# Performance work log

Hardware: AMD Instinct MI355X
Metric: run time of the kernel (lower is better)

## Reference

```python
import jax, jax.numpy as jnp
import numpy as np
from math import pi

N = 20000        # nodes
E = 640000       # edges (avg degree 32)
H = 128          # hidden_channels = num_filters
NB = 3           # num_bond_features
NGS = 50 - NB    # gaussians in smearing (num_gaussians - num_bond_features)
CUT = 10.0       # cutoff
L = 3            # num_interactions
B = 16           # graphs in batch
LOG2 = 0.6931471805599453


def ssp(x):
    # ShiftedSoftplus
    return jax.nn.softplus(x) - LOG2


def setup_inputs() -> dict:
    key = jax.random.key(0)
    ks = jax.random.split(key, 20)
    s = 0.05
    inp = {
        "z": jax.random.randint(ks[0], (N,), 0, 100),
        "pos": jax.random.uniform(ks[1], (N, 3), jnp.float32),
        "batch": jnp.sort(jax.random.randint(ks[2], (N,), 0, B)),
        "edge_index": jax.random.randint(ks[3], (2, E), 0, N),
        "edge_attr": jax.random.uniform(ks[4], (E, NB), jnp.float32),
        # parameters (stacked over L interaction blocks where per-layer)
        "emb": jax.random.normal(ks[5], (100, H), jnp.float32) * s,
        "mlp_w1": jax.random.normal(ks[6], (L, NB + NGS, H), jnp.float32) * s,
        "mlp_b1": jnp.zeros((L, H), jnp.float32),
        "mlp_w2": jax.random.normal(ks[7], (L, H, H), jnp.float32) * s,
        "mlp_b2": jnp.zeros((L, H), jnp.float32),
        "cf1_w": jax.random.normal(ks[8], (L, H, H), jnp.float32) * s,   # lin1, no bias
        "cf2_w": jax.random.normal(ks[9], (L, H, H), jnp.float32) * s,
        "cf2_b": jnp.zeros((L, H), jnp.float32),
        "lin_w": jax.random.normal(ks[10], (L, H, H), jnp.float32) * s,
        "lin_b": jnp.zeros((L, H), jnp.float32),
        "out1_w": jax.random.normal(ks[11], (H, H // 2), jnp.float32) * s,
        "out1_b": jnp.zeros((H // 2,), jnp.float32),
        "out2_w": jax.random.normal(ks[12], (H // 2, 1), jnp.float32) * s,
        "out2_b": jnp.zeros((1,), jnp.float32),
    }
    return inp


def reference(z, pos, batch, edge_index, edge_attr, emb,
              mlp_w1, mlp_b1, mlp_w2, mlp_b2,
              cf1_w, cf2_w, cf2_b, lin_w, lin_b,
              out1_w, out1_b, out2_w, out2_b):
    row, col = edge_index[0], edge_index[1]  # source j, target i
    h = emb[z]                               # [N,H] embedding_e(z)
    # edge_weight = ||pos[row] - pos[col]||
    ew = jnp.linalg.norm(pos[row] - pos[col], axis=-1)  # [E]
    # GaussianSmearing(0, cutoff, NGS)
    offset = jnp.linspace(0.0, CUT, NGS, dtype=jnp.float32)
    coeff = -0.5 / (offset[1] - offset[0]) ** 2
    gs = jnp.exp(coeff * (ew[:, None] - offset[None, :]) ** 2)  # [E,NGS]
    ea = jnp.concatenate([edge_attr, gs], axis=1)  # [E,50]
    # cosine cutoff weight
    C = 0.5 * (jnp.cos(ew * pi / CUT) + 1.0)       # [E]
    for l in range(L):
        # filter MLP on edge features
        W = ssp(ea @ mlp_w1[l] + mlp_b1[l]) @ mlp_w2[l] + mlp_b2[l]  # [E,H]
        W = W * C[:, None]
        xh = h @ cf1_w[l]                    # lin1 (no bias) [N,H]
        msg = xh[row] * W                    # gather-mul [E,H]
        agg = jax.ops.segment_sum(msg, col, num_segments=N)  # scatter-add [N,H]
        xc = agg @ cf2_w[l] + cf2_b[l]       # lin2
        xc = ssp(xc)
        xc = xc @ lin_w[l] + lin_b[l]        # block output lin
        h = h + xc                           # residual
    h = ssp(h @ out1_w + out1_b)             # [N,H/2]
    per_node = h @ out2_w + out2_b           # [N,1]
    out = jax.ops.segment_sum(per_node, batch, num_segments=B)  # readout 'add' -> [B,1]
    return out
```

## Files before the change

### kernel.cpp

```cpp
#include <hip/hip_runtime.h>
#include <hip/hip_bf16.h>

typedef __attribute__((ext_vector_type(8))) short bfrag;
typedef __attribute__((ext_vector_type(4))) float f32x4;

__device__ __forceinline__ float ssp_f(float x) {
    return fmaxf(x, 0.f) + __logf(1.f + __expf(-fabsf(x))) - 0.6931471805599453f;
}

__device__ __forceinline__ unsigned short f2b(float x) {
    __hip_bfloat16 h = __float2bfloat16(x);
    return *(unsigned short*)&h;
}

__global__ void sniff_kernel(const unsigned int* __restrict__ raw, int* __restrict__ flag)
{
    __shared__ int cnt[256];
    const int t = threadIdx.x;
    unsigned int w = raw[t];
    unsigned int e = (w >> 7) & 0xFFu;
    cnt[t] = (e >= 100u && e <= 135u) ? 1 : 0;
    __syncthreads();
    for (int s = 128; s > 0; s >>= 1) {
        if (t < s) cnt[t] += cnt[t + s];
        __syncthreads();
    }
    if (t == 0) *flag = (cnt[0] >= 160) ? 1 : 0;
}

__global__ void sniff_int_kernel(const unsigned int* __restrict__ z, int* __restrict__ iflag)
{
    __shared__ int cnt[128];
    const int t = threadIdx.x;
    cnt[t] = (z[2 * t + 1] == 0u) ? 1 : 0;
    __syncthreads();
    for (int s = 64; s > 0; s >>= 1) {
        if (t < s) cnt[t] += cnt[t + s];
        __syncthreads();
    }
    if (t == 0) *iflag = (cnt[0] >= 126) ? 1 : 0;
}

struct Cvt16 {
    const void* src[16];
    long off[17];
};

__global__ __launch_bounds__(256) void convert_fused_kernel(
    Cvt16 args, float* __restrict__ F, long total, const int* __restrict__ flag)
{
    long i = (long)blockIdx.x * 256 + threadIdx.x;
    if (i >= total) return;
    int lo = 0, hi = 16;
    while (hi - lo > 1) {
        int mid = (lo + hi) >> 1;
        if (i >= args.off[mid]) lo = mid; else hi = mid;
    }
    long loc = i - args.off[lo];
    if (*flag) F[i] = __bfloat162float(((const __hip_bfloat16*)args.src[lo])[loc]);
    else       F[i] = ((const float*)args.src[lo])[loc];
}

__global__ __launch_bounds__(256) void convert_int_kernel(
    const void* __restrict__ src, int* __restrict__ dst, int n,
    const int* __restrict__ iflag)
{
    int i = blockIdx.x * 256 + threadIdx.x;
    if (i >= n) return;
    if (*iflag) dst[i] = (int)(((const long long*)src)[i]);
    else        dst[i] = ((const int*)src)[i];
}

__global__ __launch_bounds__(256) void embed_kernel(
    const int* __restrict__ z, const float* __restrict__ embf,
    float* __restrict__ h, int NH)
{
    int idx = blockIdx.x * 256 + threadIdx.x;
    if (idx >= NH) return;
    h[idx] = embf[z[idx >> 7] * 128 + (idx & 127)];
}

__global__ __launch_bounds__(256) void zero_int_kernel(int* p, int n)
{
    int i = blockIdx.x * 256 + threadIdx.x;
    if (i < n) p[i] = 0;
}

__global__ __launch_bounds__(256) void hist_kernel(const int* __restrict__ col,
                                                   int* __restrict__ count, int E)
{
    int e = blockIdx.x * 256 + threadIdx.x;
    if (e < E) atomicAdd(&count[col[e]], 1);
}

__global__ __launch_bounds__(256) void scan_kernel(const int* __restrict__ count,
                                                   int* __restrict__ rowptr,
                                                   int* __restrict__ next, int N)
{
    __shared__ int part[256];
    const int t = threadIdx.x;
    const int chunk = (N + 255) / 256;
    const int lo = t * chunk, hi = min(lo + chunk, N);
    int s = 0;
    for (int i = lo; i < hi; ++i) s += count[i];
    part[t] = s;
    __syncthreads();
    if (t == 0) {
        int run = 0;
        for (int i = 0; i < 256; ++i) { int v = part[i]; part[i] = run; run += v; }
        rowptr[N] = run;
    }
    __syncthreads();
    int run = part[t];
    for (int i = lo; i < hi; ++i) {
        rowptr[i] = run; next[i] = run;
        run += count[i];
    }
}

__global__ __launch_bounds__(256) void slot_kernel(const int* __restrict__ col,
                                                   int* __restrict__ next,
                                                   int* __restrict__ slot, int E)
{
    int e = blockIdx.x * 256 + threadIdx.x;
    if (e < E) slot[e] = atomicAdd(&next[col[e]], 1);
}

__global__ __launch_bounds__(256) void perm_kernel(const int* __restrict__ slot,
                                                   int* __restrict__ perm, int E)
{
    int e = blockIdx.x * 256 + threadIdx.x;
    if (e < E) perm[slot[e]] = e;
}

__global__ __launch_bounds__(256) void prep_edges_kernel(
    const float* __restrict__ posf, const int* __restrict__ row,
    const int* __restrict__ col, const float* __restrict__ eattrf,
    const int* __restrict__ perm,
    int* __restrict__ rowS, int* __restrict__ colS,
    float* __restrict__ CS, float* __restrict__ ewS,
    unsigned short* __restrict__ eaS, int E, int NB)
{
    int p = blockIdx.x * 256 + threadIdx.x;
    if (p >= E) return;
    const int e = perm[p];
    const int r = row[e], c = col[e];
    float dx = posf[r*3+0] - posf[c*3+0];
    float dy = posf[r*3+1] - posf[c*3+1];
    float dz = posf[r*3+2] - posf[c*3+2];
    float ew = sqrtf(dx*dx + dy*dy + dz*dz);
    rowS[p] = r; colS[p] = c; ewS[p] = ew;
    CS[p] = 0.5f * (cosf(ew * 0.3141592653589793f) + 1.0f);
    unsigned short* o = eaS + (long)p * 4;
    for (int q = 0; q < 4; ++q)
        o[q] = (q < NB) ? f2b(eattrf[(long)e * NB + q]) : (unsigned short)0;
}

__global__ __launch_bounds__(256) void wtrans_kernel(
    const float* __restrict__ src, unsigned short* __restrict__ dst,
    int K, int Kpad, int N)
{
    int idx = blockIdx.x * 256 + threadIdx.x;
    if (idx >= N * Kpad) return;
    int n = idx / Kpad, k = idx - n * Kpad;
    dst[idx] = (k < K) ? f2b(src[k * N + n]) : (unsigned short)0;
}

__global__ __launch_bounds__(256) void wtrans_node_kernel(
    const float* __restrict__ cf1, const float* __restrict__ cf2,
    const float* __restrict__ lin, unsigned short* __restrict__ dst, int total)
{
    int idx = blockIdx.x * 256 + threadIdx.x;
    if (idx >= total) return;
    int m = idx >> 14;
    int fam = m % 3, l = m / 3;
    int local = idx & 16383;
    int n = local >> 7, k = local & 127;
    const float* src = (fam == 0 ? cf1 : fam == 1 ? cf2 : lin) + (long)l * 16384;
    dst[idx] = f2b(src[k * 128 + n]);
}

template<int MODE>
__global__ __launch_bounds__(256) void node_gemm_tiled(
    const float* __restrict__ in, const float* __restrict__ W,
    const float* __restrict__ bias, float* __restrict__ out, int N)
{
    __shared__ float in_s[32][128];
    const int t = threadIdx.x;
    const long n0 = (long)blockIdx.x * 32;
    for (int i = t; i < 32 * 128; i += 256) {
        long n = n0 + (i >> 7);
        in_s[i >> 7][i & 127] = (n < N) ? in[n * 128 + (i & 127)] : 0.f;
    }
    __syncthreads();
    const int j = t & 31, sub = t >> 5;
    const int c4 = j * 4, rb = sub * 4;
    float acc[4][4];
    float4 bv = make_float4(0.f, 0.f, 0.f, 0.f);
    if (MODE != 0) bv = *(const float4*)(bias + c4);
    #pragma unroll
    for (int i = 0; i < 4; ++i) { acc[i][0]=bv.x; acc[i][1]=bv.y; acc[i][2]=bv.z; acc[i][3]=bv.w; }
    #pragma unroll 4
    for (int k = 0; k < 128; ++k) {
        const float4 wv = *(const float4*)(W + k * 128 + c4);
        #pragma unroll
        for (int i = 0; i < 4; ++i) {
            const float a = in_s[rb + i][k];
            acc[i][0] += a * wv.x; acc[i][1] += a * wv.y;
            acc[i][2] += a * wv.z; acc[i][3] += a * wv.w;
        }
    }
    #pragma unroll
    for (int i = 0; i < 4; ++i) {
        long n = n0 + rb + i;
        if (n >= N) continue;
        float4 o;
        if (MODE == 1) {
            o.x = ssp_f(acc[i][0]); o.y = ssp_f(acc[i][1]);
            o.z = ssp_f(acc[i][2]); o.w = ssp_f(acc[i][3]);
        } else {
            o.x = acc[i][0]; o.y = acc[i][1]; o.z = acc[i][2]; o.w = acc[i][3];
        }
        if (MODE == 2) {
            float4 p = *(const float4*)(out + n * 128 + c4);
            o.x += p.x; o.y += p.y; o.z += p.z; o.w += p.w;
        }
        *(float4*)(out + n * 128 + c4) = o;
    }
}

__global__ __launch_bounds__(256) void node_gemm1_mfma(
    const float* __restrict__ in, const unsigned short* __restrict__ wt,
    float* __restrict__ out, int N)
{
    __shared__ __align__(16) short a_b[32][136];
    const int t = threadIdx.x;
    const long r0 = (long)blockIdx.x * 32;
    for (int i = t; i < 32 * 128; i += 256) {
        const int r = i >> 7, c = i & 127;
        long n = r0 + r;
        a_b[r][c] = (short)f2b((n < N) ? in[n * 128 + c] : 0.f);
    }
    __syncthreads();
    const int lane = t & 63, w = t >> 6;
    const int colL = lane & 15, quad = lane >> 4;
    const int m0 = (w & 1) * 16;
    f32x4 acc[4];
    #pragma unroll
    for (int tt = 0; tt < 4; ++tt) acc[tt] = (f32x4){0.f, 0.f, 0.f, 0.f};
    #pragma unroll
    for (int ks = 0; ks < 4; ++ks) {
        const bfrag a = *(const bfrag*)&a_b[m0 + colL][ks * 32 + quad * 8];
        #pragma unroll
        for (int tt = 0; tt < 4; ++tt) {
            const int n0 = ((w >> 1) * 4 + tt) * 16;
            const bfrag b = *(const bfrag*)&wt[(long)(n0 + colL) * 128 + ks * 32 + quad * 8];
            acc[tt] = __builtin_amdgcn_mfma_f32_16x16x32_bf16(a, b, acc[tt], 0, 0, 0);
        }
    }
    #pragma unroll
    for (int tt = 0; tt < 4; ++tt) {
        const int n0 = ((w >> 1) * 4 + tt) * 16;
        #pragma unroll
        for (int reg = 0; reg < 4; ++reg) {
            long n = r0 + m0 + quad * 4 + reg;
            if (n < N) out[n * 128 + n0 + colL] = acc[tt][reg];
        }
    }
}

__global__ __launch_bounds__(256) void node_gemm23_mfma(
    const float* __restrict__ in,
    const unsigned short* __restrict__ w1t, const float* __restrict__ b1,
    const unsigned short* __restrict__ w2t, const float* __restrict__ b2,
    float* __restrict__ h, int N)
{
    __shared__ __align__(16) short a_b[32][136];
    __shared__ __align__(16) short t_b[32][136];
    const int t = threadIdx.x;
    const long r0 = (long)blockIdx.x * 32;
    for (int i = t; i < 32 * 128; i += 256) {
        const int r = i >> 7, c = i & 127;
        long n = r0 + r;
        a_b[r][c] = (short)f2b((n < N) ? in[n * 128 + c] : 0.f);
    }
    __syncthreads();
    const int lane = t & 63, w = t >> 6;
    const int colL = lane & 15, quad = lane >> 4;
    const int m0 = (w & 1) * 16;
    {
        f32x4 acc[4];
        #pragma unroll
        for (int tt = 0; tt < 4; ++tt) acc[tt] = (f32x4){0.f, 0.f, 0.f, 0.f};
        #pragma unroll
        for (int ks = 0; ks < 4; ++ks) {
            const bfrag a = *(const bfrag*)&a_b[m0 + colL][ks * 32 + quad * 8];
            #pragma unroll
            for (int tt = 0; tt < 4; ++tt) {
                const int n0 = ((w >> 1) * 4 + tt) * 16;
                const bfrag b = *(const bfrag*)&w1t[(long)(n0 + colL) * 128 + ks * 32 + quad * 8];
                acc[tt] = __builtin_amdgcn_mfma_f32_16x16x32_bf16(a, b, acc[tt], 0, 0, 0);
            }
        }
        #pragma unroll
        for (int tt = 0; tt < 4; ++tt) {
            const int n0 = ((w >> 1) * 4 + tt) * 16;
            const float bcol = b1[n0 + colL];
            #pragma unroll
            for (int reg = 0; reg < 4; ++reg)
                t_b[m0 + quad * 4 + reg][n0 + colL] = (short)f2b(ssp_f(acc[tt][reg] + bcol));
        }
    }
    __syncthreads();
    {
        f32x4 acc[4];
        #pragma unroll
        for (int tt = 0; tt < 4; ++tt) acc[tt] = (f32x4){0.f, 0.f, 0.f, 0.f};
        #pragma unroll
        for (int ks = 0; ks < 4; ++ks) {
            const bfrag a = *(const bfrag*)&t_b[m0 + colL][ks * 32 + quad * 8];
            #pragma unroll
            for (int tt = 0; tt < 4; ++tt) {
                const int n0 = ((w >> 1) * 4 + tt) * 16;
                const bfrag b = *(const bfrag*)&w2t[(long)(n0 + colL) * 128 + ks * 32 + quad * 8];
                acc[tt] = __builtin_amdgcn_mfma_f32_16x16x32_bf16(a, b, acc[tt], 0, 0, 0);
            }
        }
        #pragma unroll
        for (int tt = 0; tt < 4; ++tt) {
            const int n0 = ((w >> 1) * 4 + tt) * 16;
            const int cg = n0 + colL;
            const float bcol = b2[cg];
            #pragma unroll
            for (int reg = 0; reg < 4; ++reg) {
                long n = r0 + m0 + quad * 4 + reg;
                if (n < N) h[n * 128 + cg] += acc[tt][reg] + bcol;
            }
        }
    }
}

__global__ __launch_bounds__(256) void edge_mfma(
    const int* __restrict__ rowS, const int* __restrict__ colS,
    const float* __restrict__ CS, const float* __restrict__ ewS,
    const unsigned short* __restrict__ eaS,
    const unsigned short* __restrict__ w1t, const float* __restrict__ b1,
    const unsigned short* __restrict__ w2t, const float* __restrict__ b2,
    const float* __restrict__ xh, float* __restrict__ agg,
    int E, int NB, int F50, float delta, float coeff)
{
    __shared__ __align__(16) short ea_b[32][64];
    __shared__ __align__(16) short t_b[32][128];
    __shared__ float runbuf[32][136];
    __shared__ int   row_s[32];
    __shared__ int   col_s[32];
    __shared__ float C_s[32];
    __shared__ float ew_s[32];
    __shared__ int   runcol_s[32];
    __shared__ int   runstart_s[33];
    __shared__ int   nruns_s;

    const int t = threadIdx.x;
    const long p0 = (long)blockIdx.x * 32;

    if (t < 32) {
        long p = p0 + t; if (p >= E) p = E - 1;
        row_s[t] = rowS[p];
        col_s[t] = colS[p];
        C_s[t]   = (p0 + t < E) ? CS[p] : 0.f;
        ew_s[t]  = ewS[p];
        if (t == 0) {
            int nr = 0;
            for (int i = 0; i < 32; ++i) {
                if (i == 0 || col_s[i] != col_s[i - 1]) {
                    runcol_s[nr] = col_s[i];
                    runstart_s[nr] = i;
                    ++nr;
                }
            }
            runstart_s[nr] = 32;
            nruns_s = nr;
        }
    }
    __syncthreads();
    for (int i = t; i < 32 * 64; i += 256) {
        const int e = i >> 6, k = i & 63;
        long p = p0 + e; if (p >= E) p = E - 1;
        unsigned short v;
        if (k < NB)        v = eaS[p * 4 + k];
        else if (k < F50) {
            float d = ew_s[e] - (float)(k - NB) * delta;
            v = f2b(__expf(coeff * d * d));
        } else             v = 0;
        ea_b[e][k] = (short)v;
    }
    __syncthreads();

    const int lane = t & 63;
    const int w    = t >> 6;
    const int colL = lane & 15;
    const int quad = lane >> 4;
    const int m0   = (w & 1) * 16;

    {
        f32x4 acc[4];
        #pragma unroll
        for (int tt = 0; tt < 4; ++tt) acc[tt] = (f32x4){0.f, 0.f, 0.f, 0.f};
        #pragma unroll
        for (int ks = 0; ks < 2; ++ks) {
            const bfrag a = *(const bfrag*)&ea_b[m0 + colL][ks * 32 + quad * 8];
            #pragma unroll
            for (int tt = 0; tt < 4; ++tt) {
                const int n0 = ((w >> 1) * 4 + tt) * 16;
                const bfrag b = *(const bfrag*)&w1t[(long)(n0 + colL) * 64 + ks * 32 + quad * 8];
                acc[tt] = __builtin_amdgcn_mfma_f32_16x16x32_bf16(a, b, acc[tt], 0, 0, 0);
            }
        }
        #pragma unroll
        for (int tt = 0; tt < 4; ++tt) {
            const int n0 = ((w >> 1) * 4 + tt) * 16;
            const float bcol = b1[n0 + colL];
            #pragma unroll
            for (int reg = 0; reg < 4; ++reg) {
                float v = ssp_f(acc[tt][reg] + bcol);
                t_b[m0 + quad * 4 + reg][n0 + colL] = (short)f2b(v);
            }
        }
    }
    __syncthreads();

    {
        f32x4 acc[4];
        #pragma unroll
        for (int tt = 0; tt < 4; ++tt) acc[tt] = (f32x4){0.f, 0.f, 0.f, 0.f};
        #pragma unroll
        for (int ks = 0; ks < 4; ++ks) {
            const bfrag a = *(const bfrag*)&t_b[m0 + colL][ks * 32 + quad * 8];
            #pragma unroll
            for (int tt = 0; tt < 4; ++tt) {
                const int n0 = ((w >> 1) * 4 + tt) * 16;
                const bfrag b = *(const bfrag*)&w2t[(long)(n0 + colL) * 128 + ks * 32 + quad * 8];
                acc[tt] = __builtin_amdgcn_mfma_f32_16x16x32_bf16(a, b, acc[tt], 0, 0, 0);
            }
        }
        const int ebase = m0 + quad * 4;
        #pragma unroll
        for (int tt = 0; tt < 4; ++tt) {
            const int n0 = ((w >> 1) * 4 + tt) * 16;
            const int cg = n0 + colL;
            const float bcol = b2[cg];
            #pragma unroll
            for (int reg = 0; reg < 4; ++reg) {
                const int e = ebase + reg;
                const float v = acc[tt][reg] + bcol;
                runbuf[e][cg] = v * C_s[e] * xh[(long)row_s[e] * 128 + cg];
            }
        }
    }
    __syncthreads();

    const int nr = nruns_s;
    const int cc = t & 127;
    for (int r = t >> 7; r < nr; r += 2) {
        float a = 0.f;
        const int s1 = runstart_s[r + 1];
        for (int e = runstart_s[r]; e < s1; ++e)
            a += runbuf[e][cc];
        atomicAdd(&agg[(long)runcol_s[r] * 128 + cc], a);
    }
}

__global__ __launch_bounds__(256) void edge_atomic(
    const float* __restrict__ posf,
    const int* __restrict__ row, const int* __restrict__ col,
    const float* __restrict__ eattrf,
    const float* __restrict__ w1, const float* __restrict__ b1,
    const float* __restrict__ w2, const float* __restrict__ b2,
    const float* __restrict__ xh, float* __restrict__ agg,
    int E, int NB, int F50, float delta, float coeff)
{
    __shared__ float ea_s[32][52];
    __shared__ float t_s[32][128];
    __shared__ int   row_s[32];
    __shared__ int   col_s[32];
    __shared__ float C_s[32];
    __shared__ float ew_s[32];

    const int t = threadIdx.x;
    const long e0 = (long)blockIdx.x * 32;

    if (t < 32) {
        long e = e0 + t; if (e >= E) e = E - 1;
        const int r = row[e], c = col[e];
        row_s[t] = r; col_s[t] = c;
        float dx = posf[r*3+0] - posf[c*3+0];
        float dy = posf[r*3+1] - posf[c*3+1];
        float dz = posf[r*3+2] - posf[c*3+2];
        float ew = sqrtf(dx*dx + dy*dy + dz*dz);
        ew_s[t] = ew;
        C_s[t]  = (e0 + t < E) ? 0.5f * (cosf(ew * 0.3141592653589793f) + 1.0f) : 0.f;
        for (int q = 0; q < NB; ++q)
            ea_s[t][q] = eattrf[e * NB + q];
    }
    __syncthreads();
    {
        const int NGS = F50 - NB;
        for (int i = t; i < 32 * NGS; i += 256) {
            const int e = i / NGS, g = i - e * NGS;
            const float d = ew_s[e] - (float)g * delta;
            ea_s[e][NB + g] = __expf(coeff * d * d);
        }
    }
    __syncthreads();

    const int j = t & 31, sub = t >> 5;
    const int c4 = j * 4, eb = sub * 4;
    float acc[4][4];
    {
        const float4 bv = *(const float4*)(b1 + c4);
        #pragma unroll
        for (int i = 0; i < 4; ++i) { acc[i][0]=bv.x; acc[i][1]=bv.y; acc[i][2]=bv.z; acc[i][3]=bv.w; }
        for (int k = 0; k < F50; ++k) {
            const float4 wv = *(const float4*)(w1 + k * 128 + c4);
            #pragma unroll
            for (int i = 0; i < 4; ++i) {
                const float a = ea_s[eb + i][k];
                acc[i][0] += a * wv.x; acc[i][1] += a * wv.y;
                acc[i][2] += a * wv.z; acc[i][3] += a * wv.w;
            }
        }
        #pragma unroll
        for (int i = 0; i < 4; ++i) {
            float4 o;
            o.x = ssp_f(acc[i][0]); o.y = ssp_f(acc[i][1]);
            o.z = ssp_f(acc[i][2]); o.w = ssp_f(acc[i][3]);
            *(float4*)&t_s[eb + i][c4] = o;
        }
    }
    __syncthreads();
    {
        const float4 bv = *(const float4*)(b2 + c4);
        #pragma unroll
        for (int i = 0; i < 4; ++i) { acc[i][0]=bv.x; acc[i][1]=bv.y; acc[i][2]=bv.z; acc[i][3]=bv.w; }
        #pragma unroll 4
        for (int k = 0; k < 128; ++k) {
            const float4 wv = *(const float4*)(w2 + k * 128 + c4);
            #pragma unroll
            for (int i = 0; i < 4; ++i) {
                const float a = t_s[eb + i][k];
                acc[i][0] += a * wv.x; acc[i][1] += a * wv.y;
                acc[i][2] += a * wv.z; acc[i][3] += a * wv.w;
            }
        }
    }
    #pragma unroll
    for (int i = 0; i < 4; ++i) {
        const int e = eb + i;
        if (e0 + e >= E) continue;
        const float Ce = C_s[e];
        const float4 xv = *(const float4*)(xh + (long)row_s[e] * 128 + c4);
        float* ag = agg + (long)col_s[e] * 128 + c4;
        atomicAdd(ag + 0, acc[i][0] * Ce * xv.x);
        atomicAdd(ag + 1, acc[i][1] * Ce * xv.y);
        atomicAdd(ag + 2, acc[i][2] * Ce * xv.z);
        atomicAdd(ag + 3, acc[i][3] * Ce * xv.w);
    }
}

__global__ __launch_bounds__(128) void readout_simple(
    const float* __restrict__ h,
    const float* __restrict__ o1w, const float* __restrict__ o1b,
    const float* __restrict__ o2w, const float* __restrict__ o2b,
    const int* __restrict__ batch, float* __restrict__ accb)
{
    __shared__ float hr[128];
    __shared__ float vv[64];
    const int n = blockIdx.x;
    const int t = threadIdx.x;
    hr[t] = h[(long)n * 128 + t];
    __syncthreads();
    if (t < 64) {
        float a = o1b[t];
        #pragma unroll 8
        for (int k = 0; k < 128; ++k)
            a = fmaf(hr[k], o1w[k * 64 + t], a);
        vv[t] = ssp_f(a) * o2w[t];
    }
    __syncthreads();
    if (t < 32) vv[t] += vv[t + 32];
    __syncthreads();
    if (t < 16) vv[t] += vv[t + 16];
    __syncthreads();
    if (t < 8)  vv[t] += vv[t + 8];
    __syncthreads();
    if (t < 4)  vv[t] += vv[t + 4];
    __syncthreads();
    if (t < 2)  vv[t] += vv[t + 2];
    __syncthreads();
    if (t == 0) atomicAdd(&accb[batch[n]], vv[0] + vv[1] + o2b[0]);
}

__global__ void finalize_kernel(const float* __restrict__ accb,
                                float* __restrict__ out, int B)
{
    int t = blockIdx.x * 256 + threadIdx.x;
    if (t < B) out[t] = accb[t];
}

extern "C" void kernel_launch(void* const* d_in, const int* in_sizes, int n_in,
                              void* d_out, int out_size, void* d_ws, size_t ws_size,
                              hipStream_t stream)
{
    const int N   = in_sizes[0];
    const int E   = in_sizes[3] / 2;
    const int B   = out_size;
    const int H   = 128;
    const int L   = in_sizes[7] / H;
    const int NB  = in_sizes[4] / E;
    const int F50 = in_sizes[6] / (L * H);
    const int NGS = F50 - NB;
    const float delta = 10.0f / (float)(NGS - 1);
    const float coeff = -0.5f / (delta * delta);

    const int fidx[16] = {1, 4, 5, 6, 7, 8, 9, 10, 11, 12, 13, 14, 15, 16, 17, 18};
    Cvt16 cv;
    cv.off[0] = 0;
    for (int i = 0; i < 16; ++i) {
        cv.src[i] = d_in[fidx[i]];
        cv.off[i + 1] = cv.off[i] + in_sizes[fidx[i]];
    }
    const long ftot = cv.off[16];

    float* F = (float*)d_ws;
    long base = (ftot + 3) & ~3L;
    float* h    = F + base;
    float* xh   = h + (long)N * H;
    float* agg  = xh + (long)N * H;
    float* accb = agg + (long)N * H;
    int*   flag  = (int*)(accb + ((B + 3) & ~3));
    int*   iflag = flag + 1;
    int*   zi     = flag + 4;
    int*   batchi = zi + N;
    int*   eidxi  = batchi + N;
    int*   count  = eidxi + 2 * E;
    int*   rowptr = count + N;
    int*   next   = rowptr + N + 1;
    int*   slot   = next + N;
    int*   perm   = slot + E;
    int*   rowS   = perm + E;
    int*   colS   = rowS + E;
    float* CS     = (float*)(colS + E);
    float* ewS    = CS + E;
    unsigned short* eaS = (unsigned short*)(ewS + E);
    unsigned short* w1t = eaS + 4L * E;
    unsigned short* w2t = w1t + (long)L * 128 * 64;
    unsigned short* nwt = w2t + (long)L * 128 * 128;
    long used_bytes = (long)((char*)(nwt + 3L * L * 128 * 128) - (char*)d_ws);
    const bool use_fast = (used_bytes <= (long)ws_size) && (F50 <= 64) && (NB <= 4);

    sniff_kernel<<<1, 256, 0, stream>>>((const unsigned int*)d_in[5], flag);
    sniff_int_kernel<<<1, 128, 0, stream>>>((const unsigned int*)d_in[0], iflag);

    convert_fused_kernel<<<(int)((ftot + 255) / 256), 256, 0, stream>>>(cv, F, ftot, flag);
    convert_int_kernel<<<(N + 255) / 256, 256, 0, stream>>>(d_in[0], zi, N, iflag);
    convert_int_kernel<<<(N + 255) / 256, 256, 0, stream>>>(d_in[2], batchi, N, iflag);
    convert_int_kernel<<<(2 * E + 255) / 256, 256, 0, stream>>>(d_in[3], eidxi, 2 * E, iflag);

    const float* posf   = F + cv.off[0];
    const float* eattrf = F + cv.off[1];
    const float* embf   = F + cv.off[2];
    const float* w1   = F + cv.off[3];  const float* b1   = F + cv.off[4];
    const float* w2   = F + cv.off[5];  const float* b2   = F + cv.off[6];
    const float* cf1  = F + cv.off[7];  const float* cf2  = F + cv.off[8];
    const float* cf2b = F + cv.off[9];  const float* lin  = F + cv.off[10];
    const float* linb = F + cv.off[11]; const float* o1   = F + cv.off[12];
    const float* o1b  = F + cv.off[13]; const float* o2   = F + cv.off[14];
    const float* o2b  = F + cv.off[15];

    if (use_fast) {
        zero_int_kernel<<<(N + 255) / 256, 256, 0, stream>>>(count, N);
        hist_kernel<<<(E + 255) / 256, 256, 0, stream>>>(eidxi + E, count, E);
        scan_kernel<<<1, 256, 0, stream>>>(count, rowptr, next, N);
        slot_kernel<<<(E + 255) / 256, 256, 0, stream>>>(eidxi + E, next, slot, E);
        perm_kernel<<<(E + 255) / 256, 256, 0, stream>>>(slot, perm, E);
        prep_edges_kernel<<<(E + 255) / 256, 256, 0, stream>>>(
            posf, eidxi, eidxi + E, eattrf, perm, rowS, colS, CS, ewS, eaS, E, NB);
        for (int l = 0; l < L; ++l) {
            wtrans_kernel<<<(128 * 64 + 255) / 256, 256, 0, stream>>>(
                w1 + (long)l * F50 * H, w1t + (long)l * 128 * 64, F50, 64, 128);
            wtrans_kernel<<<(128 * 128 + 255) / 256, 256, 0, stream>>>(
                w2 + (long)l * H * H, w2t + (long)l * 128 * 128, 128, 128, 128);
        }
        const int ntot = 3 * L * 128 * 128;
        wtrans_node_kernel<<<(ntot + 255) / 256, 256, 0, stream>>>(cf1, cf2, lin, nwt, ntot);
    }

    embed_kernel<<<(N * H + 255) / 256, 256, 0, stream>>>(zi, embf, h, N * H);
    hipMemsetAsync(accb, 0, (size_t)B * sizeof(float), stream);

    const int ngemm = (N + 31) / 32;
    const int nedge = (E + 31) / 32;
    for (int l = 0; l < L; ++l) {
        hipMemsetAsync(agg, 0, (size_t)N * H * sizeof(float), stream);
        if (use_fast) {
            node_gemm1_mfma<<<ngemm, 256, 0, stream>>>(
                h, nwt + (long)(l * 3 + 0) * 16384, xh, N);
            edge_mfma<<<nedge, 256, 0, stream>>>(
                rowS, colS, CS, ewS, eaS,
                w1t + (long)l * 128 * 64, b1 + (long)l * H,
                w2t + (long)l * 128 * 128, b2 + (long)l * H,
                xh, agg, E, NB, F50, delta, coeff);
            node_gemm23_mfma<<<ngemm, 256, 0, stream>>>(
                agg, nwt + (long)(l * 3 + 1) * 16384, cf2b + (long)l * H,
                nwt + (long)(l * 3 + 2) * 16384, linb + (long)l * H, h, N);
        } else {
            node_gemm_tiled<0><<<ngemm, 256, 0, stream>>>(h, cf1 + (long)l * H * H, nullptr, xh, N);
            edge_atomic<<<nedge, 256, 0, stream>>>(
                posf, eidxi, eidxi + E, eattrf,
                w1 + (long)l * F50 * H, b1 + (long)l * H,
                w2 + (long)l * H * H,  b2 + (long)l * H,
                xh, agg, E, NB, F50, delta, coeff);
            node_gemm_tiled<1><<<ngemm, 256, 0, stream>>>(agg, cf2 + (long)l * H * H, cf2b + (long)l * H, xh, N);
            node_gemm_tiled<2><<<ngemm, 256, 0, stream>>>(xh, lin + (long)l * H * H, linb + (long)l * H, h, N);
        }
    }

    readout_simple<<<N, 128, 0, stream>>>(h, o1, o1b, o2, o2b, batchi, accb);
    finalize_kernel<<<(B + 255) / 256, 256, 0, stream>>>(accb, (float*)d_out, B);
}
```

Before: 1.455 ms.

## Alias edge-kernel LDS buffers, swizzle bf16 tiles, and split run reduction

The edge MFMA kernel now overlays the ea/t staging buffers with the run-accumulation buffer in one shared allocation, adding a barrier before the overlay is overwritten. This cuts LDS per block so more blocks fit per CU, and the launch bounds request 8 blocks. The bf16 A-operand tiles are XOR-swizzled to reduce LDS bank conflicts. The serial single-thread run detection is replaced by each half-block scanning 16 edges and flushing an atomic whenever the target column changes, which may issue somewhat more atomics but removes a serial step.

```diff
diff --git a/kernel.cpp b/kernel.cpp
--- a/kernel.cpp
+++ b/kernel.cpp
@@ -340,7 +340,7 @@
     }
 }
 
-__global__ __launch_bounds__(256) void edge_mfma(
+__global__ __launch_bounds__(256, 8) void edge_mfma(
     const int* __restrict__ rowS, const int* __restrict__ colS,
     const float* __restrict__ CS, const float* __restrict__ ewS,
     const unsigned short* __restrict__ eaS,
@@ -349,16 +349,14 @@
     const float* __restrict__ xh, float* __restrict__ agg,
     int E, int NB, int F50, float delta, float coeff)
 {
-    __shared__ __align__(16) short ea_b[32][64];
-    __shared__ __align__(16) short t_b[32][128];
-    __shared__ float runbuf[32][136];
+    __shared__ __align__(16) char smem[32 * 132 * 4];
+    short (*ea_b)[64]    = (short(*)[64])smem;
+    short (*t_b)[128]    = (short(*)[128])(smem + 4096);
+    float (*runbuf)[132] = (float(*)[132])smem;
     __shared__ int   row_s[32];
     __shared__ int   col_s[32];
     __shared__ float C_s[32];
     __shared__ float ew_s[32];
-    __shared__ int   runcol_s[32];
-    __shared__ int   runstart_s[33];
-    __shared__ int   nruns_s;
 
     const int t = threadIdx.x;
     const long p0 = (long)blockIdx.x * 32;
@@ -369,18 +367,6 @@
         col_s[t] = colS[p];
         C_s[t]   = (p0 + t < E) ? CS[p] : 0.f;
         ew_s[t]  = ewS[p];
-        if (t == 0) {
-            int nr = 0;
-            for (int i = 0; i < 32; ++i) {
-                if (i == 0 || col_s[i] != col_s[i - 1]) {
-                    runcol_s[nr] = col_s[i];
-                    runstart_s[nr] = i;
-                    ++nr;
-                }
-            }
-            runstart_s[nr] = 32;
-            nruns_s = nr;
-        }
     }
     __syncthreads();
     for (int i = t; i < 32 * 64; i += 256) {
@@ -392,7 +378,7 @@
             float d = ew_s[e] - (float)(k - NB) * delta;
             v = f2b(__expf(coeff * d * d));
         } else             v = 0;
-        ea_b[e][k] = (short)v;
+        ea_b[e][k ^ ((e & 7) << 3)] = (short)v;
     }
     __syncthreads();
 
@@ -406,9 +392,11 @@
         f32x4 acc[4];
         #pragma unroll
         for (int tt = 0; tt < 4; ++tt) acc[tt] = (f32x4){0.f, 0.f, 0.f, 0.f};
+        const int ar  = m0 + colL;
+        const int asw = (ar & 7) << 3;
         #pragma unroll
         for (int ks = 0; ks < 2; ++ks) {
-            const bfrag a = *(const bfrag*)&ea_b[m0 + colL][ks * 32 + quad * 8];
+            const bfrag a = *(const bfrag*)&ea_b[ar][(ks * 32 + quad * 8) ^ asw];
             #pragma unroll
             for (int tt = 0; tt < 4; ++tt) {
                 const int n0 = ((w >> 1) * 4 + tt) * 16;
@@ -422,8 +410,9 @@
             const float bcol = b1[n0 + colL];
             #pragma unroll
             for (int reg = 0; reg < 4; ++reg) {
+                const int rr = m0 + quad * 4 + reg;
                 float v = ssp_f(acc[tt][reg] + bcol);
-                t_b[m0 + quad * 4 + reg][n0 + colL] = (short)f2b(v);
+                t_b[rr][(n0 + colL) ^ ((rr & 7) << 3)] = (short)f2b(v);
             }
         }
     }
@@ -433,9 +422,11 @@
         f32x4 acc[4];
         #pragma unroll
         for (int tt = 0; tt < 4; ++tt) acc[tt] = (f32x4){0.f, 0.f, 0.f, 0.f};
+        const int ar  = m0 + colL;
+        const int asw = (ar & 7) << 3;
         #pragma unroll
         for (int ks = 0; ks < 4; ++ks) {
-            const bfrag a = *(const bfrag*)&t_b[m0 + colL][ks * 32 + quad * 8];
+            const bfrag a = *(const bfrag*)&t_b[ar][(ks * 32 + quad * 8) ^ asw];
             #pragma unroll
             for (int tt = 0; tt < 4; ++tt) {
                 const int n0 = ((w >> 1) * 4 + tt) * 16;
@@ -443,6 +434,7 @@
                 acc[tt] = __builtin_amdgcn_mfma_f32_16x16x32_bf16(a, b, acc[tt], 0, 0, 0);
             }
         }
+        __syncthreads();
         const int ebase = m0 + quad * 4;
         #pragma unroll
         for (int tt = 0; tt < 4; ++tt) {
@@ -459,14 +451,21 @@
     }
     __syncthreads();
 
-    const int nr = nruns_s;
-    const int cc = t & 127;
-    for (int r = t >> 7; r < nr; r += 2) {
-        float a = 0.f;
-        const int s1 = runstart_s[r + 1];
-        for (int e = runstart_s[r]; e < s1; ++e)
+    {
+        const int cc   = t & 127;
+        const int e0h  = (t >> 7) * 16;
+        float a     = runbuf[e0h][cc];
+        int  curcol = col_s[e0h];
+        #pragma unroll 4
+        for (int e = e0h + 1; e < e0h + 16; ++e) {
+            const int c2 = col_s[e];
+            if (c2 != curcol) {
+                atomicAdd(&agg[(long)curcol * 128 + cc], a);
+                a = 0.f; curcol = c2;
+            }
             a += runbuf[e][cc];
-        atomicAdd(&agg[(long)runcol_s[r] * 128 + cc], a);
+        }
+        atomicAdd(&agg[(long)curcol * 128 + cc], a);
     }
 }
 
```

New measurement: 1.430 ms. About the same (-1.7%).
